# Kernel tuning notes

Measured on AMD Instinct MI355X. Metric: run time of the kernel, lower is better.

## Reference

```python
import jax, jax.numpy as jnp
import numpy as np

N = 100000
E = 1600000
D = 64
K = 2


def setup_inputs() -> dict:
    key = jax.random.key(0)
    k1, k2, k3 = jax.random.split(key, 3)
    x = jax.random.normal(k1, (N, D), dtype=jnp.float32)
    edge_index = jax.random.randint(k2, (2, E), 0, N, dtype=jnp.int64)
    # glorot-initialized linear: [(K+1)*D, D_out]
    fan_in, fan_out = (K + 1) * D, D
    limit = float(np.sqrt(6.0 / (fan_in + fan_out)))
    W = jax.random.uniform(k3, (fan_in, fan_out), dtype=jnp.float32, minval=-limit, maxval=limit)
    b = jnp.zeros((fan_out,), dtype=jnp.float32)
    return {"x": x, "edge_index": edge_index, "W": W, "b": b}


def reference(x, edge_index, W, b):
    n = x.shape[0]
    src = edge_index[0]
    dst = edge_index[1]
    # gcn_norm with add_self_loops=True, edge_weight=None -> ones
    loop = jnp.arange(n, dtype=src.dtype)
    src = jnp.concatenate([src, loop])
    dst = jnp.concatenate([dst, loop])
    w = jnp.ones(src.shape[0], dtype=x.dtype)
    deg = jax.ops.segment_sum(w, dst, num_segments=n)
    dinv = jnp.where(deg > 0, jax.lax.rsqrt(deg), jnp.zeros_like(deg))
    wn = dinv[src] * w * dinv[dst]  # D^-1/2 A_hat D^-1/2 edge weights
    xs = [x]
    h = x
    for _ in range(K):
        # spmm: out[i] = sum_{(j->i)} w_ji * h[j]
        h = jax.ops.segment_sum(wn[:, None] * h[src], dst, num_segments=n)
        xs.append(h)
    feats = jnp.concatenate(xs, axis=-1)  # [N, (K+1)*D]
    return feats @ W + b
```

## Files before the change

kernel.cpp:

```cpp
#include <hip/hip_runtime.h>

#define D_FEAT 64
#define CHUNK 4096
#define NBMAX 512
#define BNODES 256

typedef __attribute__((ext_vector_type(8))) short bf16x8;
typedef __attribute__((ext_vector_type(4))) float f32x4;

static __device__ inline short f2bf(float f) {
    unsigned u = __float_as_uint(f);
    u += 0x7fffu + ((u >> 16) & 1u);
    return (short)(u >> 16);
}

static __device__ inline void acc8(uint4 u, float* a) {
    a[0] += __uint_as_float(u.x << 16);
    a[1] += __uint_as_float(u.x & 0xffff0000u);
    a[2] += __uint_as_float(u.y << 16);
    a[3] += __uint_as_float(u.y & 0xffff0000u);
    a[4] += __uint_as_float(u.z << 16);
    a[5] += __uint_as_float(u.z & 0xffff0000u);
    a[6] += __uint_as_float(u.w << 16);
    a[7] += __uint_as_float(u.w & 0xffff0000u);
}

static __device__ inline uint4 pack8(const float* a, float s) {
    uint4 r;
    r.x = (unsigned)(unsigned short)f2bf(a[0] * s) | ((unsigned)(unsigned short)f2bf(a[1] * s) << 16);
    r.y = (unsigned)(unsigned short)f2bf(a[2] * s) | ((unsigned)(unsigned short)f2bf(a[3] * s) << 16);
    r.z = (unsigned)(unsigned short)f2bf(a[4] * s) | ((unsigned)(unsigned short)f2bf(a[5] * s) << 16);
    r.w = (unsigned)(unsigned short)f2bf(a[6] * s) | ((unsigned)(unsigned short)f2bf(a[7] * s) << 16);
    return r;
}


__global__ __launch_bounds__(256) void hist_kernel(const int* __restrict__ dst,
                                                   int* __restrict__ hist,
                                                   int e, int nb) {
    __shared__ int hs[NBMAX];
    int tid = threadIdx.x;
    for (int i = tid; i < nb; i += 256) hs[i] = 0;
    __syncthreads();
    int base = blockIdx.x * CHUNK;
    int end = min(base + CHUNK, e);
    for (int i = base + tid; i < end; i += 256)
        atomicAdd(&hs[dst[i] >> 8], 1);
    __syncthreads();
    for (int i = tid; i < nb; i += 256)
        hist[(size_t)blockIdx.x * nb + i] = hs[i];
}


__global__ __launch_bounds__(512) void colscan_kernel(int* __restrict__ hist,
                                                      int* __restrict__ totals,
                                                      int nc, int nb) {
    __shared__ int s[512];
    int k = blockIdx.x;
    int t = threadIdx.x;
    int v = (t < nc) ? hist[(size_t)t * nb + k] : 0;
    s[t] = v;
    __syncthreads();
    for (int off = 1; off < 512; off <<= 1) {
        int u = (t >= off) ? s[t - off] : 0;
        __syncthreads();
        s[t] += u;
        __syncthreads();
    }
    if (t < nc) hist[(size_t)t * nb + k] = s[t] - v;
    if (t == nc - 1) totals[k] = s[t];
}


__global__ __launch_bounds__(512) void base_kernel(const int* __restrict__ totals,
                                                   int* __restrict__ bbase,
                                                   int* __restrict__ rp,
                                                   int nb, int n, int e) {
    __shared__ int s[512];
    int t = threadIdx.x;
    int v = (t < nb) ? totals[t] : 0;
    s[t] = v;
    __syncthreads();
    for (int off = 1; off < 512; off <<= 1) {
        int u = (t >= off) ? s[t - off] : 0;
        __syncthreads();
        s[t] += u;
        __syncthreads();
    }
    if (t < nb) bbase[t] = s[t] - v;
    if (t == 0) {
        bbase[nb] = e;
        rp[n] = e;
    }
}


__global__ __launch_bounds__(256) void scatter_kernel(const int* __restrict__ src,
                                                      const int* __restrict__ dst,
                                                      const int* __restrict__ pref,
                                                      const int* __restrict__ bbase,
                                                      unsigned* __restrict__ pairs,
                                                      int e, int nb) {
    __shared__ int cur[NBMAX];
    int tid = threadIdx.x;
    int b = blockIdx.x;
    for (int i = tid; i < nb; i += 256)
        cur[i] = bbase[i] + pref[(size_t)b * nb + i];
    __syncthreads();
    int base = b * CHUNK;
    int end = min(base + CHUNK, e);
    for (int i = base + tid; i < end; i += 256) {
        int d = dst[i];
        int pos = atomicAdd(&cur[d >> 8], 1);
        pairs[pos] = ((unsigned)(d & 255) << 24) | (unsigned)src[i];
    }
}


__global__ __launch_bounds__(256) void csr_kernel(const unsigned* __restrict__ pairs,
                                                  const int* __restrict__ bbase,
                                                  int* __restrict__ rp,
                                                  float* __restrict__ dinv,
                                                  int* __restrict__ col, int n) {
    __shared__ int cnt[BNODES];
    __shared__ int s[BNODES];
    __shared__ int cur[BNODES];
    int tid = threadIdx.x;
    int k = blockIdx.x;
    int node0 = k * BNODES;
    int e0 = bbase[k];
    int e1 = bbase[k + 1];
    cnt[tid] = 0;
    __syncthreads();
    for (int i = e0 + tid; i < e1; i += 256)
        atomicAdd(&cnt[pairs[i] >> 24], 1);
    __syncthreads();
    int v = cnt[tid];
    s[tid] = v;
    __syncthreads();
    for (int off = 1; off < 256; off <<= 1) {
        int u = (tid >= off) ? s[tid - off] : 0;
        __syncthreads();
        s[tid] += u;
        __syncthreads();
    }
    int excl = s[tid] - v;
    cur[tid] = e0 + excl;
    int node = node0 + tid;
    if (node < n) {
        rp[node] = e0 + excl;
        dinv[node] = rsqrtf(1.0f + (float)v);
    }
    __syncthreads();
    for (int i = e0 + tid; i < e1; i += 256) {
        unsigned p = pairs[i];
        int pos = atomicAdd(&cur[p >> 24], 1);
        col[pos] = (int)(p & 0xFFFFFFu);
    }
}


__global__ __launch_bounds__(256) void convert_kernel(const float* __restrict__ x,
                                                      const float* __restrict__ dinv,
                                                      uint4* __restrict__ xb,
                                                      uint4* __restrict__ xs, int n) {
    int t = blockIdx.x * 256 + threadIdx.x;
    int node = t >> 3;
    int j = t & 7;
    if (node >= n) return;
    const float4* x4 = (const float4*)x;
    float4 a0 = x4[(size_t)node * 16 + j * 2];
    float4 a1 = x4[(size_t)node * 16 + j * 2 + 1];
    float di = dinv[node];
    float a[8] = {a0.x, a0.y, a0.z, a0.w, a1.x, a1.y, a1.z, a1.w};
    size_t o = (size_t)node * 8 + j;
    xb[o] = pack8(a, 1.0f);
    xs[o] = pack8(a, di);
}


__global__ __launch_bounds__(256) void spmm_hop1_kernel(const int* __restrict__ rp,
                                                        const int* __restrict__ col,
                                                        const float* __restrict__ dinv,
                                                        const uint4* __restrict__ xs,
                                                        uint4* __restrict__ g1b, int n) {
    int t = blockIdx.x * 256 + threadIdx.x;
    int node = t >> 3;
    int j = t & 7;
    if (node >= n) return;
    int e0 = rp[node];
    int e1 = rp[node + 1];
    float di = dinv[node];
    float a[8] = {0, 0, 0, 0, 0, 0, 0, 0};
    float c[8] = {0, 0, 0, 0, 0, 0, 0, 0};
    acc8(xs[(size_t)node * 8 + j], a);
    int e = e0;
    for (; e + 3 < e1; e += 4) {
        int s0 = col[e];
        int s1 = col[e + 1];
        int s2 = col[e + 2];
        int s3 = col[e + 3];
        uint4 u0 = xs[(size_t)s0 * 8 + j];
        uint4 u1 = xs[(size_t)s1 * 8 + j];
        uint4 u2 = xs[(size_t)s2 * 8 + j];
        uint4 u3 = xs[(size_t)s3 * 8 + j];
        acc8(u0, a);
        acc8(u1, c);
        acc8(u2, a);
        acc8(u3, c);
    }
    for (; e < e1; ++e) acc8(xs[(size_t)col[e] * 8 + j], a);
#pragma unroll
    for (int i = 0; i < 8; ++i) a[i] += c[i];
    g1b[(size_t)node * 8 + j] = pack8(a, di * di);
}


__global__ __launch_bounds__(256) void spmm_hop2_kernel(const int* __restrict__ rp,
                                                        const int* __restrict__ col,
                                                        const float* __restrict__ dinv,
                                                        const uint4* __restrict__ g1b,
                                                        uint4* __restrict__ h2b, int n) {
    int t = blockIdx.x * 256 + threadIdx.x;
    int node = t >> 3;
    int j = t & 7;
    if (node >= n) return;
    int e0 = rp[node];
    int e1 = rp[node + 1];
    float di = dinv[node];
    float a[8] = {0, 0, 0, 0, 0, 0, 0, 0};
    float c[8] = {0, 0, 0, 0, 0, 0, 0, 0};
    acc8(g1b[(size_t)node * 8 + j], a);
    int e = e0;
    for (; e + 3 < e1; e += 4) {
        int s0 = col[e];
        int s1 = col[e + 1];
        int s2 = col[e + 2];
        int s3 = col[e + 3];
        uint4 u0 = g1b[(size_t)s0 * 8 + j];
        uint4 u1 = g1b[(size_t)s1 * 8 + j];
        uint4 u2 = g1b[(size_t)s2 * 8 + j];
        uint4 u3 = g1b[(size_t)s3 * 8 + j];
        acc8(u0, a);
        acc8(u1, c);
        acc8(u2, a);
        acc8(u3, c);
    }
    for (; e < e1; ++e) acc8(g1b[(size_t)col[e] * 8 + j], a);
#pragma unroll
    for (int i = 0; i < 8; ++i) a[i] += c[i];
    h2b[(size_t)node * 8 + j] = pack8(a, di);
}


#define WT_LD 200

__global__ __launch_bounds__(256) void gemm_mfma_kernel(const unsigned short* __restrict__ xb,
                                                        const unsigned short* __restrict__ g1b,
                                                        const unsigned short* __restrict__ h2b,
                                                        const float* __restrict__ dinv,
                                                        const float* __restrict__ W,
                                                        const float* __restrict__ b,
                                                        float* __restrict__ out, int n) {
    __shared__ short sWt[64 * WT_LD];
    int tid = threadIdx.x;

    for (int i = tid; i < 192 * 64; i += 256) {
        int k = i >> 6;
        int c = i & 63;
        sWt[c * WT_LD + k] = f2bf(W[i]);
    }
    __syncthreads();

    int w = tid >> 6;
    int l = tid & 63;
    int lr = l & 15;
    int lk = l >> 4;
    int rbase = blockIdx.x * 64 + w * 16;

    int node = rbase + lr;
    int node_ld = node < n ? node : (n - 1);

    f32x4 accA[4] = {{0.f, 0.f, 0.f, 0.f}, {0.f, 0.f, 0.f, 0.f},
                     {0.f, 0.f, 0.f, 0.f}, {0.f, 0.f, 0.f, 0.f}};
    f32x4 accB[4] = {{0.f, 0.f, 0.f, 0.f}, {0.f, 0.f, 0.f, 0.f},
                     {0.f, 0.f, 0.f, 0.f}, {0.f, 0.f, 0.f, 0.f}};

    const unsigned short* srcs[3] = {xb, g1b, h2b};
#pragma unroll
    for (int kt = 0; kt < 6; ++kt) {
        const unsigned short* sp = srcs[kt >> 1];
        int kb = (kt & 1) * 32 + lk * 8;
        bf16x8 af = *(const bf16x8*)(sp + (size_t)node_ld * D_FEAT + kb);
        int kg = kt * 32 + lk * 8;
#pragma unroll
        for (int nt = 0; nt < 4; ++nt) {
            int c = nt * 16 + lr;
            bf16x8 bf = *(const bf16x8*)&sWt[c * WT_LD + kg];
            if ((kt >> 1) == 1)
                accB[nt] = __builtin_amdgcn_mfma_f32_16x16x32_bf16(af, bf, accB[nt], 0, 0, 0);
            else
                accA[nt] = __builtin_amdgcn_mfma_f32_16x16x32_bf16(af, bf, accA[nt], 0, 0, 0);
        }
    }

    float sd[4];
#pragma unroll
    for (int i = 0; i < 4; ++i) {
        int row = rbase + lk * 4 + i;
        sd[i] = (row < n) ? (1.0f / dinv[row]) : 0.0f;
    }

#pragma unroll
    for (int nt = 0; nt < 4; ++nt) {
        int c = nt * 16 + lr;
        float bias = b[c];
#pragma unroll
        for (int i = 0; i < 4; ++i) {
            int row = rbase + lk * 4 + i;
            if (row < n)
                out[(size_t)row * D_FEAT + c] = accA[nt][i] + sd[i] * accB[nt][i] + bias;
        }
    }
}


static inline size_t align256(size_t x) { return (x + 255) & ~(size_t)255; }

extern "C" void kernel_launch(void* const* d_in, const int* in_sizes, int n_in,
                              void* d_out, int out_size, void* d_ws, size_t ws_size,
                              hipStream_t stream) {
    const float* x  = (const float*)d_in[0];
    const int*   ei = (const int*)d_in[1];
    const float* W  = (const float*)d_in[2];
    const float* b  = (const float*)d_in[3];
    float* out = (float*)d_out;

    int N = in_sizes[0] / D_FEAT;
    int E = in_sizes[1] / 2;
    const int* src = ei;
    const int* dst = ei + E;

    int NB = (N + BNODES - 1) / BNODES;
    int NC = (E + CHUNK - 1) / CHUNK;

    char* base = (char*)d_ws;
    size_t off = 0;
    int* rp      = (int*)(base + off);   off = align256(off + ((size_t)N + 1) * 4);
    float* dinv  = (float*)(base + off); off = align256(off + (size_t)N * 4);
    int* totals  = (int*)(base + off);   off = align256(off + (size_t)NBMAX * 4);
    int* bbase   = (int*)(base + off);   off = align256(off + (size_t)(NBMAX + 1) * 4);
    int* col     = (int*)(base + off);   off = align256(off + (size_t)E * 4);
    uint4* xb    = (uint4*)(base + off); off = align256(off + (size_t)N * D_FEAT * 2);
    uint4* xs    = (uint4*)(base + off); off = align256(off + (size_t)N * D_FEAT * 2);
    uint4* g1b   = (uint4*)(base + off); off = align256(off + (size_t)N * D_FEAT * 2);
    uint4* h2b   = (uint4*)(base + off); off = align256(off + (size_t)N * D_FEAT * 2);
    unsigned* pairs = (unsigned*)(base + off);
    int* hist    = (int*)((char*)pairs + align256((size_t)E * 4));

    const int BS = 256;
    int gN8 = (int)(((long long)N * 8 + BS - 1) / BS);
    int gGemm = (N + 63) / 64;

    hist_kernel<<<NC, BS, 0, stream>>>(dst, hist, E, NB);
    colscan_kernel<<<NB, 512, 0, stream>>>(hist, totals, NC, NB);
    base_kernel<<<1, 512, 0, stream>>>(totals, bbase, rp, NB, N, E);
    scatter_kernel<<<NC, BS, 0, stream>>>(src, dst, hist, bbase, pairs, E, NB);
    csr_kernel<<<NB, BS, 0, stream>>>(pairs, bbase, rp, dinv, col, N);
    convert_kernel<<<gN8, BS, 0, stream>>>(x, dinv, xb, xs, N);
    spmm_hop1_kernel<<<gN8, BS, 0, stream>>>(rp, col, dinv, xs, g1b, N);
    spmm_hop2_kernel<<<gN8, BS, 0, stream>>>(rp, col, dinv, g1b, h2b, N);
    gemm_mfma_kernel<<<gGemm, BS, 0, stream>>>((const unsigned short*)xb,
                                               (const unsigned short*)g1b,
                                               (const unsigned short*)h2b,
                                               dinv, W, b, out, N);
}
```

Before: 217.3 us.

## Fuse CSR build and conversion stages into one cooperative persistent kernel

New measurement: 400.2 us. 1.84x slower.

```diff
diff --git a/kernel.cpp b/kernel.cpp
--- a/kernel.cpp
+++ b/kernel.cpp
@@ -1,9 +1,13 @@
 #include <hip/hip_runtime.h>
+#include <hip/hip_cooperative_groups.h>
+
+namespace cg = cooperative_groups;
 
 #define D_FEAT 64
 #define CHUNK 4096
 #define NBMAX 512
 #define BNODES 256
+#define GBLD 256
 
 typedef __attribute__((ext_vector_type(8))) short bf16x8;
 typedef __attribute__((ext_vector_type(4))) float f32x4;
@@ -35,147 +39,134 @@
 }
 
 
-__global__ __launch_bounds__(256) void hist_kernel(const int* __restrict__ dst,
-                                                   int* __restrict__ hist,
-                                                   int e, int nb) {
-    __shared__ int hs[NBMAX];
+__global__ __launch_bounds__(256, 2) void build_all_kernel(
+    const int* __restrict__ src, const int* __restrict__ dst,
+    const float* __restrict__ x,
+    int* __restrict__ hist,
+    int* __restrict__ totals,
+    int* __restrict__ bbase,
+    int* __restrict__ rp, float* __restrict__ dinv, int* __restrict__ col,
+    unsigned* __restrict__ pairs,
+    uint4* __restrict__ xb, uint4* __restrict__ xs,
+    int e, int n, int nb, int nc)
+{
+    cg::grid_group grid = cg::this_grid();
+    __shared__ int sh[NBMAX];
+    __shared__ int sh2[BNODES];
+    __shared__ int sh3[BNODES];
     int tid = threadIdx.x;
-    for (int i = tid; i < nb; i += 256) hs[i] = 0;
-    __syncthreads();
-    int base = blockIdx.x * CHUNK;
-    int end = min(base + CHUNK, e);
-    for (int i = base + tid; i < end; i += 256)
-        atomicAdd(&hs[dst[i] >> 8], 1);
-    __syncthreads();
-    for (int i = tid; i < nb; i += 256)
-        hist[(size_t)blockIdx.x * nb + i] = hs[i];
-}
-
-
-__global__ __launch_bounds__(512) void colscan_kernel(int* __restrict__ hist,
-                                                      int* __restrict__ totals,
-                                                      int nc, int nb) {
-    __shared__ int s[512];
-    int k = blockIdx.x;
-    int t = threadIdx.x;
-    int v = (t < nc) ? hist[(size_t)t * nb + k] : 0;
-    s[t] = v;
-    __syncthreads();
-    for (int off = 1; off < 512; off <<= 1) {
-        int u = (t >= off) ? s[t - off] : 0;
-        __syncthreads();
-        s[t] += u;
-        __syncthreads();
-    }
-    if (t < nc) hist[(size_t)t * nb + k] = s[t] - v;
-    if (t == nc - 1) totals[k] = s[t];
-}
-
-
-__global__ __launch_bounds__(512) void base_kernel(const int* __restrict__ totals,
-                                                   int* __restrict__ bbase,
-                                                   int* __restrict__ rp,
-                                                   int nb, int n, int e) {
-    __shared__ int s[512];
-    int t = threadIdx.x;
-    int v = (t < nb) ? totals[t] : 0;
-    s[t] = v;
-    __syncthreads();
-    for (int off = 1; off < 512; off <<= 1) {
-        int u = (t >= off) ? s[t - off] : 0;
-        __syncthreads();
-        s[t] += u;
-        __syncthreads();
-    }
-    if (t < nb) bbase[t] = s[t] - v;
-    if (t == 0) {
-        bbase[nb] = e;
-        rp[n] = e;
-    }
-}
-
-
-__global__ __launch_bounds__(256) void scatter_kernel(const int* __restrict__ src,
-                                                      const int* __restrict__ dst,
-                                                      const int* __restrict__ pref,
-                                                      const int* __restrict__ bbase,
-                                                      unsigned* __restrict__ pairs,
-                                                      int e, int nb) {
-    __shared__ int cur[NBMAX];
-    int tid = threadIdx.x;
-    int b = blockIdx.x;
-    for (int i = tid; i < nb; i += 256)
-        cur[i] = bbase[i] + pref[(size_t)b * nb + i];
-    __syncthreads();
-    int base = b * CHUNK;
-    int end = min(base + CHUNK, e);
-    for (int i = base + tid; i < end; i += 256) {
-        int d = dst[i];
-        int pos = atomicAdd(&cur[d >> 8], 1);
-        pairs[pos] = ((unsigned)(d & 255) << 24) | (unsigned)src[i];
-    }
-}
-
-
-__global__ __launch_bounds__(256) void csr_kernel(const unsigned* __restrict__ pairs,
-                                                  const int* __restrict__ bbase,
-                                                  int* __restrict__ rp,
-                                                  float* __restrict__ dinv,
-                                                  int* __restrict__ col, int n) {
-    __shared__ int cnt[BNODES];
-    __shared__ int s[BNODES];
-    __shared__ int cur[BNODES];
-    int tid = threadIdx.x;
-    int k = blockIdx.x;
-    int node0 = k * BNODES;
-    int e0 = bbase[k];
-    int e1 = bbase[k + 1];
-    cnt[tid] = 0;
-    __syncthreads();
-    for (int i = e0 + tid; i < e1; i += 256)
-        atomicAdd(&cnt[pairs[i] >> 24], 1);
-    __syncthreads();
-    int v = cnt[tid];
-    s[tid] = v;
-    __syncthreads();
-    for (int off = 1; off < 256; off <<= 1) {
-        int u = (tid >= off) ? s[tid - off] : 0;
-        __syncthreads();
-        s[tid] += u;
-        __syncthreads();
-    }
-    int excl = s[tid] - v;
-    cur[tid] = e0 + excl;
-    int node = node0 + tid;
-    if (node < n) {
-        rp[node] = e0 + excl;
-        dinv[node] = rsqrtf(1.0f + (float)v);
-    }
-    __syncthreads();
-    for (int i = e0 + tid; i < e1; i += 256) {
-        unsigned p = pairs[i];
-        int pos = atomicAdd(&cur[p >> 24], 1);
-        col[pos] = (int)(p & 0xFFFFFFu);
-    }
-}
-
-
-__global__ __launch_bounds__(256) void convert_kernel(const float* __restrict__ x,
-                                                      const float* __restrict__ dinv,
-                                                      uint4* __restrict__ xb,
-                                                      uint4* __restrict__ xs, int n) {
-    int t = blockIdx.x * 256 + threadIdx.x;
-    int node = t >> 3;
-    int j = t & 7;
-    if (node >= n) return;
+    int bid = blockIdx.x;
+
+    for (int c = bid; c < nc; c += GBLD) {
+        for (int i = tid; i < nb; i += 256) sh[i] = 0;
+        __syncthreads();
+        int base = c * CHUNK, end = min(base + CHUNK, e);
+        for (int i = base + tid; i < end; i += 256)
+            atomicAdd(&sh[dst[i] >> 8], 1);
+        __syncthreads();
+        for (int i = tid; i < nb; i += 256)
+            hist[(size_t)c * nb + i] = sh[i];
+        __syncthreads();
+    }
+    grid.sync();
+
+    for (int k = bid; k < nb; k += GBLD) {
+        for (int i = tid; i < 512; i += 256)
+            sh[i] = (i < nc) ? hist[(size_t)i * nb + k] : 0;
+        __syncthreads();
+        for (int off = 1; off < 512; off <<= 1) {
+            int t1 = tid + 256;
+            int v0 = (tid >= off) ? sh[tid - off] : 0;
+            int v1 = (t1 >= off) ? sh[t1 - off] : 0;
+            __syncthreads();
+            sh[tid] += v0; sh[t1] += v1;
+            __syncthreads();
+        }
+        for (int i = tid; i < nc; i += 256)
+            hist[(size_t)i * nb + k] = (i == 0) ? 0 : sh[i - 1];
+        if (tid == 0) totals[k] = sh[nc - 1];
+        __syncthreads();
+    }
+    grid.sync();
+
+    if (bid == 0) {
+        for (int i = tid; i < 512; i += 256) sh[i] = (i < nb) ? totals[i] : 0;
+        __syncthreads();
+        for (int off = 1; off < 512; off <<= 1) {
+            int t1 = tid + 256;
+            int v0 = (tid >= off) ? sh[tid - off] : 0;
+            int v1 = (t1 >= off) ? sh[t1 - off] : 0;
+            __syncthreads();
+            sh[tid] += v0; sh[t1] += v1;
+            __syncthreads();
+        }
+        for (int i = tid; i < nb; i += 256)
+            bbase[i] = (i == 0) ? 0 : sh[i - 1];
+        if (tid == 0) { bbase[nb] = e; rp[n] = e; }
+    }
+    grid.sync();
+
+    for (int c = bid; c < nc; c += GBLD) {
+        for (int i = tid; i < nb; i += 256)
+            sh[i] = bbase[i] + hist[(size_t)c * nb + i];
+        __syncthreads();
+        int base = c * CHUNK, end = min(base + CHUNK, e);
+        for (int i = base + tid; i < end; i += 256) {
+            int d = dst[i];
+            int pos = atomicAdd(&sh[d >> 8], 1);
+            pairs[pos] = ((unsigned)(d & 255) << 24) | (unsigned)src[i];
+        }
+        __syncthreads();
+    }
+    grid.sync();
+
+    for (int k = bid; k < nb; k += GBLD) {
+        int node0 = k << 8;
+        int e0 = bbase[k], e1 = bbase[k + 1];
+        sh2[tid] = 0;
+        __syncthreads();
+        for (int i = e0 + tid; i < e1; i += 256)
+            atomicAdd(&sh2[pairs[i] >> 24], 1);
+        __syncthreads();
+        int v = sh2[tid];
+        sh3[tid] = v;
+        __syncthreads();
+        for (int off = 1; off < 256; off <<= 1) {
+            int u = (tid >= off) ? sh3[tid - off] : 0;
+            __syncthreads();
+            sh3[tid] += u;
+            __syncthreads();
+        }
+        int excl = sh3[tid] - v;
+        sh[tid] = e0 + excl;
+        int node = node0 + tid;
+        if (node < n) {
+            rp[node] = e0 + excl;
+            dinv[node] = rsqrtf(1.0f + (float)v);
+        }
+        __syncthreads();
+        for (int i = e0 + tid; i < e1; i += 256) {
+            unsigned p = pairs[i];
+            int pos = atomicAdd(&sh[p >> 24], 1);
+            col[pos] = (int)(p & 0xFFFFFFu);
+        }
+        __syncthreads();
+    }
+    grid.sync();
+
+    long long total = (long long)n * 8;
     const float4* x4 = (const float4*)x;
-    float4 a0 = x4[(size_t)node * 16 + j * 2];
-    float4 a1 = x4[(size_t)node * 16 + j * 2 + 1];
-    float di = dinv[node];
-    float a[8] = {a0.x, a0.y, a0.z, a0.w, a1.x, a1.y, a1.z, a1.w};
-    size_t o = (size_t)node * 8 + j;
-    xb[o] = pack8(a, 1.0f);
-    xs[o] = pack8(a, di);
+    for (long long t = (long long)bid * 256 + tid; t < total; t += (long long)GBLD * 256) {
+        int node = (int)(t >> 3);
+        int j = (int)(t & 7);
+        float4 a0 = x4[(size_t)node * 16 + j * 2];
+        float4 a1 = x4[(size_t)node * 16 + j * 2 + 1];
+        float di = dinv[node];
+        float a[8] = {a0.x, a0.y, a0.z, a0.w, a1.x, a1.y, a1.z, a1.w};
+        size_t o = (size_t)node * 8 + j;
+        xb[o] = pack8(a, 1.0f);
+        xs[o] = pack8(a, di);
+    }
 }
 
 
@@ -362,12 +353,14 @@
     int gN8 = (int)(((long long)N * 8 + BS - 1) / BS);
     int gGemm = (N + 63) / 64;
 
-    hist_kernel<<<NC, BS, 0, stream>>>(dst, hist, E, NB);
-    colscan_kernel<<<NB, 512, 0, stream>>>(hist, totals, NC, NB);
-    base_kernel<<<1, 512, 0, stream>>>(totals, bbase, rp, NB, N, E);
-    scatter_kernel<<<NC, BS, 0, stream>>>(src, dst, hist, bbase, pairs, E, NB);
-    csr_kernel<<<NB, BS, 0, stream>>>(pairs, bbase, rp, dinv, col, N);
-    convert_kernel<<<gN8, BS, 0, stream>>>(x, dinv, xb, xs, N);
+    void* args[] = {(void*)&src, (void*)&dst, (void*)&x,
+                    (void*)&hist, (void*)&totals, (void*)&bbase,
+                    (void*)&rp, (void*)&dinv, (void*)&col,
+                    (void*)&pairs, (void*)&xb, (void*)&xs,
+                    (void*)&E, (void*)&N, (void*)&NB, (void*)&NC};
+    hipLaunchCooperativeKernel((const void*)build_all_kernel, dim3(GBLD), dim3(BS),
+                               args, 0, stream);
+
     spmm_hop1_kernel<<<gN8, BS, 0, stream>>>(rp, col, dinv, xs, g1b, N);
     spmm_hop2_kernel<<<gN8, BS, 0, stream>>>(rp, col, dinv, g1b, h2b, N);
     gemm_mfma_kernel<<<gGemm, BS, 0, stream>>>((const unsigned short*)xb,
```

## Sort nodes by degree for SpMM load balance and fuse conversion into CSR build

Applied to the files above, without the earlier changes.

Result: slower. 244.9 us (+12.7%).

```diff
diff --git a/kernel.cpp b/kernel.cpp
--- a/kernel.cpp
+++ b/kernel.cpp
@@ -36,8 +36,7 @@
 
 
 __global__ __launch_bounds__(256) void hist_kernel(const int* __restrict__ dst,
-                                                   int* __restrict__ hist,
-                                                   int e, int nb) {
+                                                   int* __restrict__ hist, int e, int nb) {
     __shared__ int hs[NBMAX];
     int tid = threadIdx.x;
     for (int i = tid; i < nb; i += 256) hs[i] = 0;
@@ -75,6 +74,7 @@
 __global__ __launch_bounds__(512) void base_kernel(const int* __restrict__ totals,
                                                    int* __restrict__ bbase,
                                                    int* __restrict__ rp,
+                                                   int* __restrict__ dbins,
                                                    int nb, int n, int e) {
     __shared__ int s[512];
     int t = threadIdx.x;
@@ -88,6 +88,7 @@
         __syncthreads();
     }
     if (t < nb) bbase[t] = s[t] - v;
+    if (t < 256) dbins[t] = 0;
     if (t == 0) {
         bbase[nb] = e;
         rp[n] = e;
@@ -117,17 +118,21 @@
 }
 
 
-__global__ __launch_bounds__(256) void csr_kernel(const unsigned* __restrict__ pairs,
-                                                  const int* __restrict__ bbase,
-                                                  int* __restrict__ rp,
-                                                  float* __restrict__ dinv,
-                                                  int* __restrict__ col, int n) {
+__global__ __launch_bounds__(256) void csr_conv_kernel(const unsigned* __restrict__ pairs,
+                                                       const int* __restrict__ bbase,
+                                                       const float* __restrict__ x,
+                                                       int* __restrict__ rp,
+                                                       float* __restrict__ dinv,
+                                                       int* __restrict__ col,
+                                                       uint4* __restrict__ xb,
+                                                       uint4* __restrict__ xs, int n) {
     __shared__ int cnt[BNODES];
     __shared__ int s[BNODES];
     __shared__ int cur[BNODES];
+    __shared__ float sdv[BNODES];
     int tid = threadIdx.x;
     int k = blockIdx.x;
-    int node0 = k * BNODES;
+    int node0 = k << 8;
     int e0 = bbase[k];
     int e1 = bbase[k + 1];
     cnt[tid] = 0;
@@ -146,10 +151,12 @@
     }
     int excl = s[tid] - v;
     cur[tid] = e0 + excl;
+    float dv = rsqrtf(1.0f + (float)v);
+    sdv[tid] = dv;
     int node = node0 + tid;
     if (node < n) {
         rp[node] = e0 + excl;
-        dinv[node] = rsqrtf(1.0f + (float)v);
+        dinv[node] = dv;
     }
     __syncthreads();
     for (int i = e0 + tid; i < e1; i += 256) {
@@ -157,37 +164,88 @@
         int pos = atomicAdd(&cur[p >> 24], 1);
         col[pos] = (int)(p & 0xFFFFFFu);
     }
-}
-
-
-__global__ __launch_bounds__(256) void convert_kernel(const float* __restrict__ x,
-                                                      const float* __restrict__ dinv,
-                                                      uint4* __restrict__ xb,
-                                                      uint4* __restrict__ xs, int n) {
-    int t = blockIdx.x * 256 + threadIdx.x;
-    int node = t >> 3;
-    int j = t & 7;
-    if (node >= n) return;
     const float4* x4 = (const float4*)x;
-    float4 a0 = x4[(size_t)node * 16 + j * 2];
-    float4 a1 = x4[(size_t)node * 16 + j * 2 + 1];
-    float di = dinv[node];
-    float a[8] = {a0.x, a0.y, a0.z, a0.w, a1.x, a1.y, a1.z, a1.w};
-    size_t o = (size_t)node * 8 + j;
-    xb[o] = pack8(a, 1.0f);
-    xs[o] = pack8(a, di);
-}
-
-
-__global__ __launch_bounds__(256) void spmm_hop1_kernel(const int* __restrict__ rp,
+    for (int t = tid; t < BNODES * 8; t += 256) {
+        int nl = t >> 3;
+        int j = t & 7;
+        int nd = node0 + nl;
+        if (nd < n) {
+            float4 a0 = x4[(size_t)nd * 16 + j * 2];
+            float4 a1 = x4[(size_t)nd * 16 + j * 2 + 1];
+            float di = sdv[nl];
+            float a[8] = {a0.x, a0.y, a0.z, a0.w, a1.x, a1.y, a1.z, a1.w};
+            size_t o = (size_t)nd * 8 + j;
+            xb[o] = pack8(a, 1.0f);
+            xs[o] = pack8(a, di);
+        }
+    }
+}
+
+
+__global__ __launch_bounds__(256) void deghist_kernel(const int* __restrict__ rp,
+                                                      int* __restrict__ dbins, int n) {
+    __shared__ int hs[256];
+    int tid = threadIdx.x;
+    hs[tid] = 0;
+    __syncthreads();
+    int i = blockIdx.x * 256 + tid;
+    if (i < n) {
+        int d = rp[i + 1] - rp[i];
+        atomicAdd(&hs[d > 255 ? 255 : d], 1);
+    }
+    __syncthreads();
+    if (hs[tid]) atomicAdd(&dbins[tid], hs[tid]);
+}
+
+__global__ __launch_bounds__(256) void degbase_kernel(const int* __restrict__ dbins,
+                                                      int* __restrict__ dcur) {
+    __shared__ int s[256];
+    int tid = threadIdx.x;
+    int v = dbins[tid];
+    s[tid] = v;
+    __syncthreads();
+    for (int off = 1; off < 256; off <<= 1) {
+        int u = (tid >= off) ? s[tid - off] : 0;
+        __syncthreads();
+        s[tid] += u;
+        __syncthreads();
+    }
+    dcur[tid] = s[tid] - v;
+}
+
+__global__ __launch_bounds__(256) void degplace_kernel(const int* __restrict__ rp,
+                                                       int* __restrict__ dcur,
+                                                       int* __restrict__ perm, int n) {
+    __shared__ int hs[256];
+    __shared__ int base[256];
+    int tid = threadIdx.x;
+    hs[tid] = 0;
+    __syncthreads();
+    int i = blockIdx.x * 256 + tid;
+    int bin = 0, off = 0;
+    if (i < n) {
+        int d = rp[i + 1] - rp[i];
+        bin = d > 255 ? 255 : d;
+        off = atomicAdd(&hs[bin], 1);
+    }
+    __syncthreads();
+    if (hs[tid]) base[tid] = atomicAdd(&dcur[tid], hs[tid]);
+    __syncthreads();
+    if (i < n) perm[base[bin] + off] = i;
+}
+
+
+__global__ __launch_bounds__(256) void spmm_hop1_kernel(const int* __restrict__ perm,
+                                                        const int* __restrict__ rp,
                                                         const int* __restrict__ col,
                                                         const float* __restrict__ dinv,
                                                         const uint4* __restrict__ xs,
                                                         uint4* __restrict__ g1b, int n) {
     int t = blockIdx.x * 256 + threadIdx.x;
-    int node = t >> 3;
+    int nidx = t >> 3;
     int j = t & 7;
-    if (node >= n) return;
+    if (nidx >= n) return;
+    int node = perm[nidx];
     int e0 = rp[node];
     int e1 = rp[node + 1];
     float di = dinv[node];
@@ -216,15 +274,17 @@
 }
 
 
-__global__ __launch_bounds__(256) void spmm_hop2_kernel(const int* __restrict__ rp,
+__global__ __launch_bounds__(256) void spmm_hop2_kernel(const int* __restrict__ perm,
+                                                        const int* __restrict__ rp,
                                                         const int* __restrict__ col,
                                                         const float* __restrict__ dinv,
                                                         const uint4* __restrict__ g1b,
                                                         uint4* __restrict__ h2b, int n) {
     int t = blockIdx.x * 256 + threadIdx.x;
-    int node = t >> 3;
+    int nidx = t >> 3;
     int j = t & 7;
-    if (node >= n) return;
+    if (nidx >= n) return;
+    int node = perm[nidx];
     int e0 = rp[node];
     int e1 = rp[node + 1];
     float di = dinv[node];
@@ -350,6 +410,9 @@
     float* dinv  = (float*)(base + off); off = align256(off + (size_t)N * 4);
     int* totals  = (int*)(base + off);   off = align256(off + (size_t)NBMAX * 4);
     int* bbase   = (int*)(base + off);   off = align256(off + (size_t)(NBMAX + 1) * 4);
+    int* dbins   = (int*)(base + off);   off = align256(off + 256 * 4);
+    int* dcur    = (int*)(base + off);   off = align256(off + 256 * 4);
+    int* perm    = (int*)(base + off);   off = align256(off + (size_t)N * 4);
     int* col     = (int*)(base + off);   off = align256(off + (size_t)E * 4);
     uint4* xb    = (uint4*)(base + off); off = align256(off + (size_t)N * D_FEAT * 2);
     uint4* xs    = (uint4*)(base + off); off = align256(off + (size_t)N * D_FEAT * 2);
@@ -359,17 +422,20 @@
     int* hist    = (int*)((char*)pairs + align256((size_t)E * 4));
 
     const int BS = 256;
+    int gN1 = (N + BS - 1) / BS;
     int gN8 = (int)(((long long)N * 8 + BS - 1) / BS);
     int gGemm = (N + 63) / 64;
 
     hist_kernel<<<NC, BS, 0, stream>>>(dst, hist, E, NB);
     colscan_kernel<<<NB, 512, 0, stream>>>(hist, totals, NC, NB);
-    base_kernel<<<1, 512, 0, stream>>>(totals, bbase, rp, NB, N, E);
+    base_kernel<<<1, 512, 0, stream>>>(totals, bbase, rp, dbins, NB, N, E);
     scatter_kernel<<<NC, BS, 0, stream>>>(src, dst, hist, bbase, pairs, E, NB);
-    csr_kernel<<<NB, BS, 0, stream>>>(pairs, bbase, rp, dinv, col, N);
-    convert_kernel<<<gN8, BS, 0, stream>>>(x, dinv, xb, xs, N);
-    spmm_hop1_kernel<<<gN8, BS, 0, stream>>>(rp, col, dinv, xs, g1b, N);
-    spmm_hop2_kernel<<<gN8, BS, 0, stream>>>(rp, col, dinv, g1b, h2b, N);
+    csr_conv_kernel<<<NB, BS, 0, stream>>>(pairs, bbase, x, rp, dinv, col, xb, xs, N);
+    deghist_kernel<<<gN1, BS, 0, stream>>>(rp, dbins, N);
+    degbase_kernel<<<1, BS, 0, stream>>>(dbins, dcur);
+    degplace_kernel<<<gN1, BS, 0, stream>>>(rp, dcur, perm, N);
+    spmm_hop1_kernel<<<gN8, BS, 0, stream>>>(perm, rp, col, dinv, xs, g1b, N);
+    spmm_hop2_kernel<<<gN8, BS, 0, stream>>>(perm, rp, col, dinv, g1b, h2b, N);
     gemm_mfma_kernel<<<gGemm, BS, 0, stream>>>((const unsigned short*)xb,
                                                (const unsigned short*)g1b,
                                                (const unsigned short*)h2b,
```
